# Kernel tuning notes

Hardware: AMD Instinct MI355X
Metric: run time of the kernel (lower is better)

The kernel has to match this reference:

```python
import jax, jax.numpy as jnp
import numpy as np

NEG_BIG = 1e30  # matches the 1e+30 masking constant in the original


def setup_inputs() -> dict:
    key = jax.random.key(0)
    ks = jax.random.split(key, 6)
    B, Lc, Lq, D = 8, 512, 64, 256
    return {
        "context": jax.random.normal(ks[0], (B, Lc, D), jnp.float32),
        "question": jax.random.normal(ks[1], (B, Lq, D), jnp.float32),
        "mask": jnp.ones((B, Lq), jnp.int32),
        "att_w": jax.random.normal(ks[2], (3 * D,), jnp.float32) * 0.05,  # Linear(6H=3D -> 1) weight
        "att_b": jnp.zeros((1,), jnp.float32),                            # Linear bias
        "w_in": jax.random.normal(ks[3], (D,), jnp.float32) * 0.05,       # input_linear (no bias)
        "w_mem": jax.random.normal(ks[4], (D,), jnp.float32) * 0.05,      # memory_linear (no bias)
    }


def reference(context, question, mask, att_w, att_b, w_in, w_mem):
    # context: [B,Lc,D], question: [B,Lq,D], mask: [B,Lq] (0/1)
    D = context.shape[-1]
    # Separable (mathematically identical) form of Linear(cat([c, q, c*q])):
    # score[b,i,j] = c_i . w_c + q_j . w_q + sum_d c[b,i,d]*q[b,j,d]*w_p[d] + b
    w_c, w_q, w_p = att_w[:D], att_w[D:2 * D], att_w[2 * D:]
    sc = jnp.einsum('bid,d->bi', context, w_c)                 # [B,Lc]
    sq = jnp.einsum('bjd,d->bj', question, w_q)                # [B,Lq]
    sp = jnp.einsum('bid,bjd->bij', context * w_p, question)   # [B,Lc,Lq]
    attention = sc[:, :, None] + sq[:, None, :] + sp + att_b[0]

    maskf = mask.astype(attention.dtype)
    masked = attention - NEG_BIG * (1.0 - maskf)[:, None, :]   # [B,Lc,Lq]

    ctx1 = jnp.einsum('bid,d->bi', context, w_in)[..., None]   # input_linear:  [B,Lc,1]
    q1 = jnp.einsum('bjd,d->bj', question, w_mem)[..., None]   # memory_linear: [B,Lq,1]

    h_aware_weight = jax.nn.softmax(masked, axis=-1)           # [B,Lc,Lq]
    U = jnp.matmul(h_aware_weight, q1)                         # [B,Lc,1]

    u_aware_weight = jax.nn.softmax(jnp.max(masked, axis=-1), axis=-1)[:, None, :]  # [B,1,Lc]
    H = jnp.matmul(u_aware_weight, ctx1)                       # [B,1,1]

    G = jnp.concatenate([ctx1, U, ctx1 * U, U * H], axis=-1)   # [B,Lc,4]
    return G
```

## Files before the change

### kernel.cpp

```cpp
#include <hip/hip_runtime.h>

#define NB 8
#define LC 512
#define LQ 64
#define DD 256
#define NEG_BIG_F 1e30f

#define TPB 512
#define RPW 2
#define RPB 16
#define BPB (LC / RPB)

__device__ __forceinline__ float bcastf(float x, int lane) {
  return __uint_as_float((unsigned)__builtin_amdgcn_readlane((int)__float_as_uint(x), lane));
}

__global__ __launch_bounds__(TPB) void rows_kernel(
    const float* __restrict__ context,
    const float* __restrict__ question,
    const int*   __restrict__ mask,
    const float* __restrict__ att_w,
    const float* __restrict__ att_b,
    const float* __restrict__ w_in,
    const float* __restrict__ w_mem,
    float* __restrict__ out,
    float* __restrict__ ws)
{
  __shared__ float4 qs4[64][64];
  __shared__ float sq_part[LQ][8];
  __shared__ float q1_part[LQ][8];
  __shared__ float sqm[LQ];
  __shared__ float q1s[LQ];

  const int tid  = threadIdx.x;
  const int b    = blockIdx.x / BPB;
  const int row0 = (blockIdx.x % BPB) * RPB;

  {
    const int j  = tid >> 3;
    const int dq = tid & 7;
    const float4* qrow = (const float4*)(question + ((size_t)b * LQ + j) * DD + dq * 32);
    const float4* wq   = (const float4*)(att_w + DD + dq * 32);
    const float4* wm   = (const float4*)(w_mem + dq * 32);
    float psq = 0.f, pq1 = 0.f;
#pragma unroll
    for (int k = 0; k < 8; ++k) {
      float4 v = qrow[k];
      float4 a = wq[k];
      float4 c = wm[k];
      psq += v.x*a.x + v.y*a.y + v.z*a.z + v.w*a.w;
      pq1 += v.x*c.x + v.y*c.y + v.z*c.z + v.w*c.w;
      qs4[dq*8 + k][j] = v;
    }
    sq_part[j][dq] = psq;
    q1_part[j][dq] = pq1;
  }
  __syncthreads();
  if (tid < LQ) {
    const int j = tid;
    float sq = att_b[0];
    float q1 = 0.f;
#pragma unroll
    for (int k = 0; k < 8; ++k) { sq += sq_part[j][k]; q1 += q1_part[j][k]; }
    float mf = (float)mask[b * LQ + j];
    sqm[j] = sq - NEG_BIG_F * (1.0f - mf);
    q1s[j] = q1;
  }
  __syncthreads();

  const int w  = tid >> 6;
  const int l  = tid & 63;
  const int i0 = row0 + w * RPW;

  const float4 wc4 = ((const float4*)att_w)[l];
  const float4 wp4 = ((const float4*)(att_w + 2 * DD))[l];
  const float4 wi4 = ((const float4*)w_in)[l];

  float4 cp[RPW];
  float sc[RPW], c1[RPW];
#pragma unroll
  for (int r = 0; r < RPW; ++r) {
    float4 c4 = ((const float4*)(context + ((size_t)b * LC + i0 + r) * DD))[l];
    sc[r] = c4.x*wc4.x + c4.y*wc4.y + c4.z*wc4.z + c4.w*wc4.w;
    c1[r] = c4.x*wi4.x + c4.y*wi4.y + c4.z*wi4.z + c4.w*wi4.w;
    cp[r].x = c4.x*wp4.x; cp[r].y = c4.y*wp4.y; cp[r].z = c4.z*wp4.z; cp[r].w = c4.w*wp4.w;
  }
#pragma unroll
  for (int off = 32; off > 0; off >>= 1) {
#pragma unroll
    for (int r = 0; r < RPW; ++r) {
      sc[r] += __shfl_xor(sc[r], off);
      c1[r] += __shfl_xor(c1[r], off);
    }
  }

  float acc[RPW] = {0.f, 0.f};
#pragma unroll
  for (int c = 0; c < 64; ++c) {
    float4 qv = qs4[c][l];
#pragma unroll
    for (int r = 0; r < RPW; ++r) {
      acc[r] += bcastf(cp[r].x, c) * qv.x
              + bcastf(cp[r].y, c) * qv.y
              + bcastf(cp[r].z, c) * qv.z
              + bcastf(cp[r].w, c) * qv.w;
    }
  }

  const float sqm_l = sqm[l];
  const float q1_l  = q1s[l];
#pragma unroll
  for (int r = 0; r < RPW; ++r) {
    float v = acc[r] + sc[r] + sqm_l;
    float m = v;
#pragma unroll
    for (int off = 32; off > 0; off >>= 1) m = fmaxf(m, __shfl_xor(m, off));
    float p  = __expf(v - m);
    float ps = p;
    float pu = p * q1_l;
#pragma unroll
    for (int off = 32; off > 0; off >>= 1) {
      ps += __shfl_xor(ps, off);
      pu += __shfl_xor(pu, off);
    }
    if (l == 0) {
      const int gi = b * LC + i0 + r;
      const float U = pu / ps;
      out[gi * 4 + 0] = c1[r];
      out[gi * 4 + 1] = U;
      out[gi * 4 + 2] = c1[r] * U;
      ws[gi]               = m;
      ws[NB * LC + gi]     = c1[r];
      ws[2 * NB * LC + gi] = U;
    }
  }
}

__global__ __launch_bounds__(512) void batch_kernel(
    const float* __restrict__ ws,
    float* __restrict__ out)
{
  const int b = blockIdx.x;
  const int t = threadIdx.x;
  const int gi = b * LC + t;
  const float m  = ws[gi];
  const float c1 = ws[NB * LC + gi];
  const float U  = ws[2 * NB * LC + gi];

  const int w = t >> 6, l = t & 63;
  __shared__ float rmax[8], rs[8], rc[8];

  float mx = m;
#pragma unroll
  for (int off = 32; off > 0; off >>= 1) mx = fmaxf(mx, __shfl_xor(mx, off));
  if (l == 0) rmax[w] = mx;
  __syncthreads();
  mx = rmax[0];
#pragma unroll
  for (int k = 1; k < 8; ++k) mx = fmaxf(mx, rmax[k]);

  float p  = __expf(m - mx);
  float ps = p;
  float pc = p * c1;
#pragma unroll
  for (int off = 32; off > 0; off >>= 1) {
    ps += __shfl_xor(ps, off);
    pc += __shfl_xor(pc, off);
  }
  if (l == 0) { rs[w] = ps; rc[w] = pc; }
  __syncthreads();
  float S = 0.f, C = 0.f;
#pragma unroll
  for (int k = 0; k < 8; ++k) { S += rs[k]; C += rc[k]; }

  const float H = C / S;
  out[gi * 4 + 3] = U * H;
}

extern "C" void kernel_launch(void* const* d_in, const int* in_sizes, int n_in,
                              void* d_out, int out_size, void* d_ws, size_t ws_size,
                              hipStream_t stream) {
  const float* context  = (const float*)d_in[0];
  const float* question = (const float*)d_in[1];
  const int*   mask     = (const int*)d_in[2];
  const float* att_w    = (const float*)d_in[3];
  const float* att_b    = (const float*)d_in[4];
  const float* w_in     = (const float*)d_in[5];
  const float* w_mem    = (const float*)d_in[6];
  float* out = (float*)d_out;
  float* ws  = (float*)d_ws;

  rows_kernel<<<dim3(NB * BPB), dim3(TPB), 0, stream>>>(
      context, question, mask, att_w, att_b, w_in, w_mem, out, ws);
  batch_kernel<<<dim3(NB), dim3(512), 0, stream>>>(ws, out);
}
```

Measured before the change: 89.60 us.

## Halve rows-kernel block size, prefetch context rows, pack workspace and outputs as float4

The rows kernel now runs 4 waves of 256 threads, each handling 4 context rows, and loads those rows at kernel start so the reads overlap with question staging. The question preprocessing is remapped to one wave per 64-wide slice of the feature dimension. Intermediates (m, c1, U) go to the workspace as one float4 per row, and the batch kernel writes all four output columns with a single float4 store, replacing scattered scalar writes. The tradeoff is more registers and serial work per wave, with fewer waves per block to hide latency.

```diff
diff --git a/kernel.cpp b/kernel.cpp
--- a/kernel.cpp
+++ b/kernel.cpp
@@ -6,8 +6,9 @@
 #define DD 256
 #define NEG_BIG_F 1e30f
 
-#define TPB 512
-#define RPW 2
+#define TPB 256
+#define NWAVE 4
+#define RPW 4
 #define RPB 16
 #define BPB (LC / RPB)
 
@@ -23,37 +24,45 @@
     const float* __restrict__ att_b,
     const float* __restrict__ w_in,
     const float* __restrict__ w_mem,
-    float* __restrict__ out,
-    float* __restrict__ ws)
+    float4* __restrict__ ws4)
 {
   __shared__ float4 qs4[64][64];
-  __shared__ float sq_part[LQ][8];
-  __shared__ float q1_part[LQ][8];
+  __shared__ float sq_part[LQ][NWAVE + 1];
+  __shared__ float q1_part[LQ][NWAVE + 1];
   __shared__ float sqm[LQ];
   __shared__ float q1s[LQ];
 
   const int tid  = threadIdx.x;
+  const int w    = tid >> 6;
+  const int l    = tid & 63;
   const int b    = blockIdx.x / BPB;
   const int row0 = (blockIdx.x % BPB) * RPB;
+  const int i0   = row0 + w * RPW;
+
+  const float4 wc4 = ((const float4*)att_w)[l];
+  const float4 wp4 = ((const float4*)(att_w + 2 * DD))[l];
+  const float4 wi4 = ((const float4*)w_in)[l];
+  float4 c4r[RPW];
+#pragma unroll
+  for (int r = 0; r < RPW; ++r)
+    c4r[r] = ((const float4*)(context + ((size_t)b * LC + i0 + r) * DD))[l];
 
   {
-    const int j  = tid >> 3;
-    const int dq = tid & 7;
-    const float4* qrow = (const float4*)(question + ((size_t)b * LQ + j) * DD + dq * 32);
-    const float4* wq   = (const float4*)(att_w + DD + dq * 32);
-    const float4* wm   = (const float4*)(w_mem + dq * 32);
+    const float4* qrow = (const float4*)(question + ((size_t)b * LQ + l) * DD + w * 64);
+    const float4* wqp  = (const float4*)(att_w + DD + w * 64);
+    const float4* wmp  = (const float4*)(w_mem + w * 64);
     float psq = 0.f, pq1 = 0.f;
 #pragma unroll
-    for (int k = 0; k < 8; ++k) {
+    for (int k = 0; k < 16; ++k) {
       float4 v = qrow[k];
-      float4 a = wq[k];
-      float4 c = wm[k];
+      float4 a = wqp[k];
+      float4 c = wmp[k];
       psq += v.x*a.x + v.y*a.y + v.z*a.z + v.w*a.w;
       pq1 += v.x*c.x + v.y*c.y + v.z*c.z + v.w*c.w;
-      qs4[dq*8 + k][j] = v;
+      qs4[w * 16 + k][l] = v;
     }
-    sq_part[j][dq] = psq;
-    q1_part[j][dq] = pq1;
+    sq_part[l][w] = psq;
+    q1_part[l][w] = pq1;
   }
   __syncthreads();
   if (tid < LQ) {
@@ -61,26 +70,18 @@
     float sq = att_b[0];
     float q1 = 0.f;
 #pragma unroll
-    for (int k = 0; k < 8; ++k) { sq += sq_part[j][k]; q1 += q1_part[j][k]; }
+    for (int k = 0; k < NWAVE; ++k) { sq += sq_part[j][k]; q1 += q1_part[j][k]; }
     float mf = (float)mask[b * LQ + j];
     sqm[j] = sq - NEG_BIG_F * (1.0f - mf);
     q1s[j] = q1;
   }
   __syncthreads();
 
-  const int w  = tid >> 6;
-  const int l  = tid & 63;
-  const int i0 = row0 + w * RPW;
-
-  const float4 wc4 = ((const float4*)att_w)[l];
-  const float4 wp4 = ((const float4*)(att_w + 2 * DD))[l];
-  const float4 wi4 = ((const float4*)w_in)[l];
-
   float4 cp[RPW];
   float sc[RPW], c1[RPW];
 #pragma unroll
   for (int r = 0; r < RPW; ++r) {
-    float4 c4 = ((const float4*)(context + ((size_t)b * LC + i0 + r) * DD))[l];
+    float4 c4 = c4r[r];
     sc[r] = c4.x*wc4.x + c4.y*wc4.y + c4.z*wc4.z + c4.w*wc4.w;
     c1[r] = c4.x*wi4.x + c4.y*wi4.y + c4.z*wi4.z + c4.w*wi4.w;
     cp[r].x = c4.x*wp4.x; cp[r].y = c4.y*wp4.y; cp[r].z = c4.z*wp4.z; cp[r].w = c4.w*wp4.w;
@@ -94,7 +95,7 @@
     }
   }
 
-  float acc[RPW] = {0.f, 0.f};
+  float acc[RPW] = {0.f, 0.f, 0.f, 0.f};
 #pragma unroll
   for (int c = 0; c < 64; ++c) {
     float4 qv = qs4[c][l];
@@ -125,27 +126,20 @@
     }
     if (l == 0) {
       const int gi = b * LC + i0 + r;
-      const float U = pu / ps;
-      out[gi * 4 + 0] = c1[r];
-      out[gi * 4 + 1] = U;
-      out[gi * 4 + 2] = c1[r] * U;
-      ws[gi]               = m;
-      ws[NB * LC + gi]     = c1[r];
-      ws[2 * NB * LC + gi] = U;
+      ws4[gi] = make_float4(m, c1[r], pu / ps, 0.f);
     }
   }
 }
 
 __global__ __launch_bounds__(512) void batch_kernel(
-    const float* __restrict__ ws,
-    float* __restrict__ out)
+    const float4* __restrict__ ws4,
+    float4* __restrict__ out4)
 {
-  const int b = blockIdx.x;
-  const int t = threadIdx.x;
+  const int b  = blockIdx.x;
+  const int t  = threadIdx.x;
   const int gi = b * LC + t;
-  const float m  = ws[gi];
-  const float c1 = ws[NB * LC + gi];
-  const float U  = ws[2 * NB * LC + gi];
+  const float4 v = ws4[gi];
+  const float m = v.x, c1 = v.y, U = v.z;
 
   const int w = t >> 6, l = t & 63;
   __shared__ float rmax[8], rs[8], rc[8];
@@ -174,7 +168,7 @@
   for (int k = 0; k < 8; ++k) { S += rs[k]; C += rc[k]; }
 
   const float H = C / S;
-  out[gi * 4 + 3] = U * H;
+  out4[gi] = make_float4(c1, U, c1 * U, U * H);
 }
 
 extern "C" void kernel_launch(void* const* d_in, const int* in_sizes, int n_in,
@@ -187,10 +181,10 @@
   const float* att_b    = (const float*)d_in[4];
   const float* w_in     = (const float*)d_in[5];
   const float* w_mem    = (const float*)d_in[6];
-  float* out = (float*)d_out;
-  float* ws  = (float*)d_ws;
+  float4* out4 = (float4*)d_out;
+  float4* ws4  = (float4*)d_ws;
 
   rows_kernel<<<dim3(NB * BPB), dim3(TPB), 0, stream>>>(
-      context, question, mask, att_w, att_b, w_in, w_mem, out, ws);
-  batch_kernel<<<dim3(NB), dim3(512), 0, stream>>>(ws, out);
+      context, question, mask, att_w, att_b, w_in, w_mem, ws4);
+  batch_kernel<<<dim3(NB), dim3(512), 0, stream>>>(ws4, out4);
 }
```

After: 85.06 us. -5.1%, faster.
